# Kernel optimization log

Measured on AMD Instinct MI355X. Metric: run time of the kernel, lower is better.

The kernel has to match this reference:

```python
import jax, jax.numpy as jnp
import numpy as np

N_NODES, SEQ_LEN, IN_CH, HID, OUT_CH, N_EDGES = 10000, 12, 16, 64, 1, 160000


def setup_inputs() -> dict:
    key = jax.random.key(0)
    ks = jax.random.split(key, 16)
    s = 1.0 / np.sqrt(HID)
    u = lambda k, shape: jax.random.uniform(k, shape, jnp.float32, -s, s)
    return {
        "x_seq": jax.random.normal(ks[0], (1, SEQ_LEN, N_NODES, IN_CH), jnp.float32),
        "edge_index": jax.random.randint(ks[1], (2, N_EDGES), 0, N_NODES, jnp.int32),
        "gcn_w": jax.random.normal(ks[2], (IN_CH, HID), jnp.float32) / np.sqrt(IN_CH),
        "gcn_b": jnp.zeros((HID,), jnp.float32),
        "w_ih0": u(ks[3], (3 * HID, HID)),
        "w_hh0": u(ks[4], (3 * HID, HID)),
        "b_ih0": u(ks[5], (3 * HID,)),
        "b_hh0": u(ks[6], (3 * HID,)),
        "w_ih1": u(ks[7], (3 * HID, HID)),
        "w_hh1": u(ks[8], (3 * HID, HID)),
        "b_ih1": u(ks[9], (3 * HID,)),
        "b_hh1": u(ks[10], (3 * HID,)),
        "attn_w": u(ks[11], (HID, 1)),
        "attn_b": u(ks[12], (1,)),
        "fc_w": u(ks[13], (HID, OUT_CH)),
        "fc_b": u(ks[14], (OUT_CH,)),
    }


def _gcn_all_t(x_ntf, edge_index, w, b):
    # x_ntf: (N, T, F). Symmetric-normalized GCNConv with self loops (PyG default),
    # applied to every timestep at once (edge structure is static).
    n = x_ntf.shape[0]
    loop = jnp.arange(n, dtype=edge_index.dtype)
    src = jnp.concatenate([edge_index[0], loop])
    dst = jnp.concatenate([edge_index[1], loop])
    deg = jax.ops.segment_sum(jnp.ones_like(src, dtype=x_ntf.dtype), dst, num_segments=n)
    dis = jax.lax.rsqrt(deg)  # deg >= 1 thanks to self loops
    norm = dis[src] * dis[dst]  # (E+N,)
    msg = x_ntf[src] * norm[:, None, None]  # (E+N, T, F)
    agg = jax.ops.segment_sum(msg, dst, num_segments=n)  # (N, T, F)
    return agg @ w + b  # (N, T, H)


def _gru_layer(x, w_ih, w_hh, b_ih, b_hh):
    # x: (B, T, Hin) batch_first; PyTorch GRU cell equations, h0 = 0.
    bsz, _, _ = x.shape
    h_dim = w_hh.shape[1]
    xi = x @ w_ih.T + b_ih  # (B, T, 3H), precomputed input projections

    def step(h, xt):
        gh = h @ w_hh.T + b_hh
        ir, iz, in_ = jnp.split(xt, 3, axis=-1)
        hr, hz, hn = jnp.split(gh, 3, axis=-1)
        r = jax.nn.sigmoid(ir + hr)
        z = jax.nn.sigmoid(iz + hz)
        n = jnp.tanh(in_ + r * hn)
        h_new = (1.0 - z) * n + z * h
        return h_new, h_new

    h0 = jnp.zeros((bsz, h_dim), x.dtype)
    _, hs = jax.lax.scan(step, h0, jnp.swapaxes(xi, 0, 1))  # (T, B, H)
    return jnp.swapaxes(hs, 0, 1)


def reference(x_seq, edge_index, gcn_w, gcn_b, w_ih0, w_hh0, b_ih0, b_hh0,
              w_ih1, w_hh1, b_ih1, b_hh1, attn_w, attn_b, fc_w, fc_b):
    batch, seq_len, num_nodes, _ = x_seq.shape  # batch == 1 (see notes)
    # (B, T, N, F) -> (N, T, F)
    x_ntf = jnp.swapaxes(x_seq[0], 0, 1)
    gcn_out = jax.nn.relu(_gcn_all_t(x_ntf, edge_index, gcn_w, gcn_b))  # (N, T, H)
    # gru_input: (B*N, T, H); dropout between GRU layers disabled (inference)
    h1 = _gru_layer(gcn_out, w_ih0, w_hh0, b_ih0, b_hh0)
    gru_out = _gru_layer(h1, w_ih1, w_hh1, b_ih1, b_hh1)  # (N, T, H)
    attn_scores = jax.nn.softmax(gru_out @ attn_w + attn_b, axis=1)  # (N, T, 1)
    context = jnp.sum(attn_scores * gru_out, axis=1)  # (N, H)
    residual = (context @ fc_w + fc_b).reshape(batch, num_nodes, -1)
    last_known = x_seq[:, -1, :, 0][..., None]  # (B, N, 1)
    return last_known + residual
```

## Files before the change

### kernel.cpp

```cpp
#include <hip/hip_runtime.h>
#include <hip/hip_bf16.h>

#define N_NODES 10000
#define SEQ_T 12
#define IN_CH 16
#define HID 64
#define N_EDGES 160000
#define CAP 96
#define PB 0xAAAAAAAAu

typedef __attribute__((ext_vector_type(8))) short short8;
typedef __attribute__((ext_vector_type(4))) float floatx4;

__device__ __forceinline__ float frcp(float x){ return __builtin_amdgcn_rcpf(x); }
__device__ __forceinline__ float sigmf(float x){ return frcp(1.0f + __expf(-x)); }
__device__ __forceinline__ float tanh_fast(float x){ return 1.0f - 2.0f * frcp(1.0f + __expf(2.0f * x)); }
__device__ __forceinline__ unsigned short f2bf(float f){
  union { float f; unsigned int u; } c; c.f = f;
  unsigned int u = c.u;
  return (unsigned short)((u + 0x7FFFu + ((u >> 16) & 1u)) >> 16);
}


__global__ void k_fill(const int* __restrict__ ei, unsigned int* __restrict__ cnt,
                       int* __restrict__ csr,
                       const float* __restrict__ wih0, const float* __restrict__ whh0,
                       const float* __restrict__ wih1, const float* __restrict__ whh1,
                       unsigned short* __restrict__ wF){
  int i = blockIdx.x * 256 + threadIdx.x;
  if (i < 49152){
    const float* srcs[4] = {wih0, whh0, wih1, whh1};
    int p = i / 12288, ii = i - p * 12288;
    int e = ii & 7, l = (ii >> 3) & 63, jk = ii >> 9;
    int kt = jk / 12, jt = jk - kt * 12;
    int j = (l & 15) + 16 * jt;
    int k = ((l >> 4) * 8) + e + 32 * kt;
    wF[i] = f2bf(srcs[p][j * 64 + k]);
  }
  int s = ei[i], d = ei[N_EDGES + i];
  unsigned int pos = atomicAdd(&cnt[d], 1u) - PB;
  if (pos < CAP) csr[d * CAP + pos] = s;
}

__global__ __launch_bounds__(256, 3) void k_fused(
    const float* __restrict__ x, const unsigned int* __restrict__ cnt,
    const int* __restrict__ csr,
    const float* __restrict__ gcn_w, const float* __restrict__ gcn_b,
    const unsigned short* __restrict__ wF,
    const float* __restrict__ bih0, const float* __restrict__ bhh0,
    const float* __restrict__ bih1, const float* __restrict__ bhh1,
    const float* __restrict__ attn_w, const float* __restrict__ fc_w,
    const float* __restrict__ fc_b, float* __restrict__ out){
  __shared__ union {
    struct {
      float sm[SEQ_T][16][17];
      float smw[IN_CH * HID];
      float smb[HID];
      int2  eLDS[16][16];
    } A;
    struct {
      unsigned short HL[SEQ_T][1024];
      float scdc[SEQ_T][2][16];
    } B;
  } U;
  __shared__ union {
    unsigned short gout[SEQ_T][1024];
    unsigned short h1[2][1024];
  } V;

  const int tid = threadIdx.x;
  const int blk = blockIdx.x;

  {
    for (int i = tid; i < IN_CH * HID; i += 256) U.A.smw[i] = gcn_w[i];
    if (tid < HID) U.A.smb[tid] = gcn_b[tid];
    const int g = tid >> 4, ch = tid & 15;
    const int dst = blk * 16 + g;
    int deg = (int)(cnt[dst] - PB);
    if (deg > CAP) deg = CAP;
    float selfdis = rsqrtf((float)deg + 1.0f);
    float acc[SEQ_T];
    #pragma unroll
    for (int t = 0; t < SEQ_T; ++t)
      acc[t] = selfdis * x[((size_t)t * N_NODES + dst) * IN_CH + ch];
    for (int base = 0; base < deg; base += 16){
      int ep = base + ch;
      int2 ev = make_int2(0, 0);
      if (ep < deg){
        int s = csr[dst * CAP + ep];
        ev = make_int2(s, __float_as_int(rsqrtf((float)(cnt[s] - PB) + 1.0f)));
      }
      U.A.eLDS[g][ch] = ev;
      int c2 = deg - base; if (c2 > 16) c2 = 16;
      #pragma unroll 4
      for (int j = 0; j < c2; ++j){
        int2 e2 = U.A.eLDS[g][j];
        float wgt = __int_as_float(e2.y);
        const float* xp = x + (size_t)e2.x * IN_CH + ch;
        #pragma unroll
        for (int t = 0; t < SEQ_T; ++t)
          acc[t] = fmaf(wgt, xp[(size_t)t * N_NODES * IN_CH], acc[t]);
      }
    }
    #pragma unroll
    for (int t = 0; t < SEQ_T; ++t) U.A.sm[t][g][ch] = selfdis * acc[t];
    __syncthreads();
    const int hq = tid & 15;
    float wreg[16][4];
    #pragma unroll
    for (int f = 0; f < 16; ++f)
      #pragma unroll
      for (int j = 0; j < 4; ++j) wreg[f][j] = U.A.smw[f * HID + hq * 4 + j];
    float b0 = U.A.smb[hq * 4],     b1 = U.A.smb[hq * 4 + 1],
          b2 = U.A.smb[hq * 4 + 2], b3 = U.A.smb[hq * 4 + 3];
    const int lb = (hq >> 3) * 512 + (g + 16 * ((hq >> 1) & 3)) * 8 + (hq & 1) * 4;
    #pragma unroll
    for (int t = 0; t < SEQ_T; ++t){
      float o0 = b0, o1 = b1, o2 = b2, o3 = b3;
      #pragma unroll
      for (int f = 0; f < 16; ++f){
        float v = U.A.sm[t][g][f];
        o0 = fmaf(v, wreg[f][0], o0);
        o1 = fmaf(v, wreg[f][1], o1);
        o2 = fmaf(v, wreg[f][2], o2);
        o3 = fmaf(v, wreg[f][3], o3);
      }
      ushort4 ov;
      ov.x = f2bf(fmaxf(o0, 0.0f));
      ov.y = f2bf(fmaxf(o1, 0.0f));
      ov.z = f2bf(fmaxf(o2, 0.0f));
      ov.w = f2bf(fmaxf(o3, 0.0f));
      *(ushort4*)(&V.gout[t][lb]) = ov;
    }
    __syncthreads();
  }

  const int w = tid >> 6;
  const int l = tid & 63;
  const int c = l & 15;
  const int q = l >> 4;
  const int hb = w * 16 + c;
  const int kt_h = hb >> 5;
  const int e_h = hb & 7;
  const int lf_h = 16 * ((hb >> 3) & 3);

  {
    float brz = bih0[hb] + bhh0[hb];
    float bzz = bih0[64 + hb] + bhh0[64 + hb];
    float bin = bih0[128 + hb], bhn = bhh0[128 + hb];
    short8 bw[2][3][2];
    #pragma unroll
    for (int g2 = 0; g2 < 2; ++g2)
      #pragma unroll
      for (int s = 0; s < 3; ++s)
        #pragma unroll
        for (int kt = 0; kt < 2; ++kt){
          int jt = w + 4 * s;
          size_t idx = ((((size_t)g2 * 2 + kt) * 12 + jt) * 64 + l) * 8;
          bw[g2][s][kt] = *(const short8*)(wF + idx);
        }
    float hp[4] = {0.f, 0.f, 0.f, 0.f};
    for (int t = 0; t < SEQ_T; ++t){
      short8 xa[2], ha[2];
      #pragma unroll
      for (int kt = 0; kt < 2; ++kt)
        xa[kt] = *(const short8*)&V.gout[t][kt * 512 + l * 8];
      if (t > 0){
        #pragma unroll
        for (int kt = 0; kt < 2; ++kt)
          ha[kt] = *(const short8*)&U.B.HL[t - 1][(kt * 64 + l) * 8];
      }
      floatx4 acc[2][3];
      #pragma unroll
      for (int g2 = 0; g2 < 2; ++g2)
        #pragma unroll
        for (int s = 0; s < 3; ++s) acc[g2][s] = (floatx4){0.f, 0.f, 0.f, 0.f};
      #pragma unroll
      for (int s = 0; s < 3; ++s)
        #pragma unroll
        for (int kt = 0; kt < 2; ++kt)
          acc[0][s] = __builtin_amdgcn_mfma_f32_16x16x32_bf16(xa[kt], bw[0][s][kt], acc[0][s], 0, 0, 0);
      if (t > 0){
        #pragma unroll
        for (int s = 0; s < 3; ++s)
          #pragma unroll
          for (int kt = 0; kt < 2; ++kt)
            acc[1][s] = __builtin_amdgcn_mfma_f32_16x16x32_bf16(ha[kt], bw[1][s][kt], acc[1][s], 0, 0, 0);
      }
      #pragma unroll
      for (int r = 0; r < 4; ++r){
        float rr = sigmf(acc[0][0][r] + acc[1][0][r] + brz);
        float zz = sigmf(acc[0][1][r] + acc[1][1][r] + bzz);
        float nn = tanh_fast(acc[0][2][r] + bin + rr * (acc[1][2][r] + bhn));
        float hn = (1.0f - zz) * nn + zz * hp[r];
        hp[r] = hn;
        U.B.HL[t][(kt_h * 64 + (q * 4 + r) + lf_h) * 8 + e_h] = f2bf(hn);
      }
      __syncthreads();
    }
  }

  short8 bwA[2];
  #pragma unroll
  for (int kt = 0; kt < 2; ++kt){
    short8 v;
    #pragma unroll
    for (int e = 0; e < 8; ++e){
      int k = q * 8 + e + 32 * kt;
      float f = (c == 0) ? attn_w[k] : (c == 1) ? fc_w[k] : 0.0f;
      v[e] = (short)f2bf(f);
    }
    bwA[kt] = v;
  }

  {
    float brz = bih1[hb] + bhh1[hb];
    float bzz = bih1[64 + hb] + bhh1[64 + hb];
    float bin = bih1[128 + hb], bhn = bhh1[128 + hb];
    short8 bw[2][3][2];
    #pragma unroll
    for (int g2 = 0; g2 < 2; ++g2)
      #pragma unroll
      for (int s = 0; s < 3; ++s)
        #pragma unroll
        for (int kt = 0; kt < 2; ++kt){
          int jt = w + 4 * s;
          size_t idx = ((((size_t)(2 + g2) * 2 + kt) * 12 + jt) * 64 + l) * 8;
          bw[g2][s][kt] = *(const short8*)(wF + idx);
        }
    float hp[4] = {0.f, 0.f, 0.f, 0.f};
    for (int t = 0; t < SEQ_T; ++t){
      int pr = t & 1;
      short8 xa[2], ha[2];
      #pragma unroll
      for (int kt = 0; kt < 2; ++kt)
        xa[kt] = *(const short8*)&U.B.HL[t][(kt * 64 + l) * 8];
      if (t > 0){
        #pragma unroll
        for (int kt = 0; kt < 2; ++kt)
          ha[kt] = *(const short8*)&V.h1[pr][(kt * 64 + l) * 8];
      }
      floatx4 acc[2][3];
      #pragma unroll
      for (int g2 = 0; g2 < 2; ++g2)
        #pragma unroll
        for (int s = 0; s < 3; ++s) acc[g2][s] = (floatx4){0.f, 0.f, 0.f, 0.f};
      #pragma unroll
      for (int s = 0; s < 3; ++s)
        #pragma unroll
        for (int kt = 0; kt < 2; ++kt)
          acc[0][s] = __builtin_amdgcn_mfma_f32_16x16x32_bf16(xa[kt], bw[0][s][kt], acc[0][s], 0, 0, 0);
      if (t > 0){
        #pragma unroll
        for (int s = 0; s < 3; ++s)
          #pragma unroll
          for (int kt = 0; kt < 2; ++kt)
            acc[1][s] = __builtin_amdgcn_mfma_f32_16x16x32_bf16(ha[kt], bw[1][s][kt], acc[1][s], 0, 0, 0);
      }
      if (w == 0 && t >= 1){
        floatx4 aA = (floatx4){0.f, 0.f, 0.f, 0.f};
        #pragma unroll
        for (int kt = 0; kt < 2; ++kt)
          aA = __builtin_amdgcn_mfma_f32_16x16x32_bf16(ha[kt], bwA[kt], aA, 0, 0, 0);
        if (c < 2){
          #pragma unroll
          for (int r = 0; r < 4; ++r) U.B.scdc[t - 1][c][q * 4 + r] = aA[r];
        }
      }
      #pragma unroll
      for (int r = 0; r < 4; ++r){
        float rr = sigmf(acc[0][0][r] + acc[1][0][r] + brz);
        float zz = sigmf(acc[0][1][r] + acc[1][1][r] + bzz);
        float nn = tanh_fast(acc[0][2][r] + bin + rr * (acc[1][2][r] + bhn));
        float hn = (1.0f - zz) * nn + zz * hp[r];
        hp[r] = hn;
        V.h1[1 - pr][(kt_h * 64 + (q * 4 + r) + lf_h) * 8 + e_h] = f2bf(hn);
      }
      __syncthreads();
    }
  }

  if (w == 0){
    short8 hL[2];
    #pragma unroll
    for (int kt = 0; kt < 2; ++kt)
      hL[kt] = *(const short8*)&V.h1[0][(kt * 64 + l) * 8];
    floatx4 aA = (floatx4){0.f, 0.f, 0.f, 0.f};
    #pragma unroll
    for (int kt = 0; kt < 2; ++kt)
      aA = __builtin_amdgcn_mfma_f32_16x16x32_bf16(hL[kt], bwA[kt], aA, 0, 0, 0);
    if (c < 2){
      #pragma unroll
      for (int r = 0; r < 4; ++r) U.B.scdc[SEQ_T - 1][c][q * 4 + r] = aA[r];
    }
    int gn = blk * 16 + l;
    if (l < 16){
      float sc[SEQ_T], dc[SEQ_T];
      #pragma unroll
      for (int t = 0; t < SEQ_T; ++t){ sc[t] = U.B.scdc[t][0][l]; dc[t] = U.B.scdc[t][1][l]; }
      float m = sc[0];
      #pragma unroll
      for (int t = 1; t < SEQ_T; ++t) m = fmaxf(m, sc[t]);
      float den = 0.0f, num = 0.0f;
      #pragma unroll
      for (int t = 0; t < SEQ_T; ++t){
        float p = __expf(sc[t] - m);
        den += p;
        num = fmaf(p, dc[t], num);
      }
      float y = fc_b[0] + num * frcp(den);
      float last = x[((size_t)(SEQ_T - 1) * N_NODES + gn) * IN_CH];
      out[gn] = last + y;
    }
  }
}

extern "C" void kernel_launch(void* const* d_in, const int* in_sizes, int n_in,
                              void* d_out, int out_size, void* d_ws, size_t ws_size,
                              hipStream_t stream){
  const float* x = (const float*)d_in[0];
  const int* ei  = (const int*)d_in[1];
  char* ws = (char*)d_ws;
  unsigned int*   cnt = (unsigned int*)(ws);
  int*            csr = (int*)(ws + 40960);
  unsigned short* wF  = (unsigned short*)(ws + 3880960);

  k_fill<<<625, 256, 0, stream>>>(ei, cnt, csr,
      (const float*)d_in[4], (const float*)d_in[5],
      (const float*)d_in[8], (const float*)d_in[9], wF);
  k_fused<<<625, 256, 0, stream>>>(
      x, cnt, csr,
      (const float*)d_in[2], (const float*)d_in[3], wF,
      (const float*)d_in[6],  (const float*)d_in[7],
      (const float*)d_in[10], (const float*)d_in[11],
      (const float*)d_in[12], (const float*)d_in[14], (const float*)d_in[15],
      (float*)d_out);
}
```

Baseline: 160.0 us.

## Pre-transpose node features to node-major fp16 layout for GCN gather

The fill kernel now also writes a node-major copy of x in fp16, storing all 12 timesteps of each channel contiguously. The GCN aggregation then gathers each neighbor's row with three 8-byte loads instead of 12 strided fp32 loads spaced a full timestep apart. This aims to cut scattered memory traffic and gather latency in the edge loop. In exchange it adds an extra transposition pass and lowers the input features to half precision.

```diff
diff --git a/kernel.cpp b/kernel.cpp
--- a/kernel.cpp
+++ b/kernel.cpp
@@ -20,13 +20,23 @@
   unsigned int u = c.u;
   return (unsigned short)((u + 0x7FFFu + ((u >> 16) & 1u)) >> 16);
 }
+__device__ __forceinline__ unsigned short f2h(float f){
+  _Float16 h = (_Float16)f; unsigned short u; __builtin_memcpy(&u, &h, 2); return u;
+}
+__device__ __forceinline__ float h2f(unsigned short u){
+  _Float16 h; __builtin_memcpy(&h, &u, 2); return (float)h;
+}
+__device__ __forceinline__ void cvt4(ushort4 v, float* o){
+  o[0] = h2f(v.x); o[1] = h2f(v.y); o[2] = h2f(v.z); o[3] = h2f(v.w);
+}
 
 
 __global__ void k_fill(const int* __restrict__ ei, unsigned int* __restrict__ cnt,
                        int* __restrict__ csr,
                        const float* __restrict__ wih0, const float* __restrict__ whh0,
                        const float* __restrict__ wih1, const float* __restrict__ whh1,
-                       unsigned short* __restrict__ wF){
+                       unsigned short* __restrict__ wF,
+                       const float* __restrict__ x, unsigned short* __restrict__ xT){
   int i = blockIdx.x * 256 + threadIdx.x;
   if (i < 49152){
     const float* srcs[4] = {wih0, whh0, wih1, whh1};
@@ -37,14 +47,25 @@
     int k = ((l >> 4) * 8) + e + 32 * kt;
     wF[i] = f2bf(srcs[p][j * 64 + k]);
   }
+  {
+    int n = i >> 4, ch = i & 15;
+    const float* xp = x + (size_t)n * IN_CH + ch;
+    unsigned short tmp[SEQ_T];
+    #pragma unroll
+    for (int t = 0; t < SEQ_T; ++t) tmp[t] = f2h(xp[(size_t)t * N_NODES * IN_CH]);
+    unsigned short* dp = xT + (size_t)n * 192 + ch * 12;
+    *(ushort4*)(dp)     = make_ushort4(tmp[0], tmp[1], tmp[2],  tmp[3]);
+    *(ushort4*)(dp + 4) = make_ushort4(tmp[4], tmp[5], tmp[6],  tmp[7]);
+    *(ushort4*)(dp + 8) = make_ushort4(tmp[8], tmp[9], tmp[10], tmp[11]);
+  }
   int s = ei[i], d = ei[N_EDGES + i];
   unsigned int pos = atomicAdd(&cnt[d], 1u) - PB;
   if (pos < CAP) csr[d * CAP + pos] = s;
 }
 
 __global__ __launch_bounds__(256, 3) void k_fused(
-    const float* __restrict__ x, const unsigned int* __restrict__ cnt,
-    const int* __restrict__ csr,
+    const float* __restrict__ x, const unsigned short* __restrict__ xT,
+    const unsigned int* __restrict__ cnt, const int* __restrict__ csr,
     const float* __restrict__ gcn_w, const float* __restrict__ gcn_b,
     const unsigned short* __restrict__ wF,
     const float* __restrict__ bih0, const float* __restrict__ bhh0,
@@ -80,9 +101,15 @@
     if (deg > CAP) deg = CAP;
     float selfdis = rsqrtf((float)deg + 1.0f);
     float acc[SEQ_T];
-    #pragma unroll
-    for (int t = 0; t < SEQ_T; ++t)
-      acc[t] = selfdis * x[((size_t)t * N_NODES + dst) * IN_CH + ch];
+    {
+      const unsigned short* xs = xT + (size_t)dst * 192 + ch * 12;
+      float f[SEQ_T];
+      cvt4(*(const ushort4*)(xs),     f);
+      cvt4(*(const ushort4*)(xs + 4), f + 4);
+      cvt4(*(const ushort4*)(xs + 8), f + 8);
+      #pragma unroll
+      for (int t = 0; t < SEQ_T; ++t) acc[t] = selfdis * f[t];
+    }
     for (int base = 0; base < deg; base += 16){
       int ep = base + ch;
       int2 ev = make_int2(0, 0);
@@ -96,10 +123,15 @@
       for (int j = 0; j < c2; ++j){
         int2 e2 = U.A.eLDS[g][j];
         float wgt = __int_as_float(e2.y);
-        const float* xp = x + (size_t)e2.x * IN_CH + ch;
+        const unsigned short* xp = xT + (size_t)e2.x * 192 + ch * 12;
+        ushort4 va = *(const ushort4*)(xp);
+        ushort4 vb = *(const ushort4*)(xp + 4);
+        ushort4 vc = *(const ushort4*)(xp + 8);
+        float f[SEQ_T];
+        cvt4(va, f); cvt4(vb, f + 4); cvt4(vc, f + 8);
         #pragma unroll
         for (int t = 0; t < SEQ_T; ++t)
-          acc[t] = fmaf(wgt, xp[(size_t)t * N_NODES * IN_CH], acc[t]);
+          acc[t] = fmaf(wgt, f[t], acc[t]);
       }
     }
     #pragma unroll
@@ -324,12 +356,14 @@
   unsigned int*   cnt = (unsigned int*)(ws);
   int*            csr = (int*)(ws + 40960);
   unsigned short* wF  = (unsigned short*)(ws + 3880960);
+  unsigned short* xT  = (unsigned short*)(ws + 3979264);
 
   k_fill<<<625, 256, 0, stream>>>(ei, cnt, csr,
       (const float*)d_in[4], (const float*)d_in[5],
-      (const float*)d_in[8], (const float*)d_in[9], wF);
+      (const float*)d_in[8], (const float*)d_in[9], wF,
+      x, xT);
   k_fused<<<625, 256, 0, stream>>>(
-      x, cnt, csr,
+      x, xT, cnt, csr,
       (const float*)d_in[2], (const float*)d_in[3], wF,
       (const float*)d_in[6],  (const float*)d_in[7],
       (const float*)d_in[10], (const float*)d_in[11],
```

Measured after the change: 141.2 us. 11.7% less time.
